# Kernel optimization log

Measured on AMD Instinct MI355X. Metric: run time of the kernel, lower is better.

## Reference

```python
import jax, jax.numpy as jnp
from jax import lax
import numpy as np

I, H, B, S = 512, 1024, 64, 512


def setup_inputs() -> dict:
    key = jax.random.key(0)
    ks = jax.random.split(key, 10)
    xav = lambda k, shape: jax.random.uniform(k, shape, jnp.float32, -1.0, 1.0) * jnp.sqrt(6.0 / (shape[0] + shape[1]))
    return {
        "x": jax.random.normal(ks[0], (B, S, I), jnp.float32),
        "wii": xav(ks[1], (I, H)), "bii": jnp.zeros((H,), jnp.float32),
        "whi": xav(ks[2], (H, H)), "bhi": jnp.zeros((H,), jnp.float32),
        "wif": xav(ks[3], (I, H)), "bif": jnp.zeros((H,), jnp.float32),
        "whf": xav(ks[4], (H, H)), "bhf": jnp.zeros((H,), jnp.float32),
        "wig": xav(ks[5], (I, H)), "big": jnp.zeros((H,), jnp.float32),
        "whg": xav(ks[6], (H, H)), "bhg": jnp.zeros((H,), jnp.float32),
        "wio": xav(ks[7], (I, H)), "bio": jnp.zeros((H,), jnp.float32),
        "who": xav(ks[8], (H, H)), "bho": jnp.zeros((H,), jnp.float32),
    }


def reference(x, wii, bii, whi, bhi, wif, bif, whf, bhf,
              wig, big, whg, bhg, wio, bio, who, bho):
    b, s, _ = x.shape
    h = wii.shape[1]
    # Fuse the four per-gate GEMMs into single (I,4H) / (H,4H) GEMMs — same math.
    Wx = jnp.concatenate([wii, wif, wig, wio], axis=1)   # (I, 4H)
    Wh = jnp.concatenate([whi, whf, whg, who], axis=1)   # (H, 4H)
    bb = jnp.concatenate([bii + bhi, bif + bhf, big + bhg, bio + bho])  # (4H,)
    xs = jnp.swapaxes(x, 0, 1)                            # (S, B, I)
    x_proj = jnp.einsum('sbi,ik->sbk', xs, Wx) + bb       # (S, B, 4H)

    def step(carry, xp):
        h_t, c_t = carry
        gates = xp + h_t @ Wh                             # (B, 4H)
        i_t, f_t, g_t, o_t = jnp.split(gates, 4, axis=-1)
        i_t = jax.nn.sigmoid(i_t)
        f_t = jax.nn.sigmoid(f_t)
        g_t = jnp.tanh(g_t)
        o_t = jax.nn.sigmoid(o_t)
        c_t = f_t * c_t + i_t * g_t
        h_t = o_t * jnp.tanh(c_t)
        return (h_t, c_t), None

    h0 = jnp.zeros((b, h), x.dtype)
    c0 = jnp.zeros((b, h), x.dtype)
    (h_T, c_T), _ = lax.scan(step, (h0, c0), x_proj)
    return (h_T, c_T)
```

## Files before the change

### kernel.cpp

```cpp
#include <hip/hip_runtime.h>
#include <hip/hip_bf16.h>
#include <stdint.h>

typedef __bf16 bf16_t;
typedef bf16_t bf16x8 __attribute__((ext_vector_type(8)));
typedef float  f32x4  __attribute__((ext_vector_type(4)));
typedef float  f32x16 __attribute__((ext_vector_type(16)));

#define I_DIM 512
#define H_DIM 1024
#define B_DIM 64
#define S_DIM 512
#define G4    4096
#define CHUNK 16
#define NCHUNK (S_DIM / CHUNK)
#define XPSLOT_ELEMS ((size_t)CHUNK * 64 * G4)

#define O_WXT   0x0000000ULL
#define O_WHTF  0x0400000ULL
#define O_BIAS  0x0C00000ULL
#define O_HBUF  0x0D00000ULL
#define O_BAR   0x0D40000ULL
#define O_XP    0x1200000ULL

#define XPD_IDX(c)  (2048 + (c) * 64)
#define CONS_IDX(c) (4096 + (c) * 64)
#define QF_BASE     6144

__device__ __forceinline__ float sigm(float x)      { return 1.f / (1.f + __expf(-x)); }
__device__ __forceinline__ float tanh_fast(float x) { return 1.f - 2.f / (__expf(2.f * x) + 1.f); }


__global__ void k_pack_wx(const float* __restrict__ w0, const float* __restrict__ w1,
                          const float* __restrict__ w2, const float* __restrict__ w3,
                          bf16_t* __restrict__ wxt) {
    int tid = blockIdx.x * 256 + threadIdx.x;
    int k = tid >> 12;
    int p = tid & 4095;
    int q = p >> 5, g = (p >> 3) & 3, jj = p & 7;
    int j = q * 8 + jj;
    const float* src = (g == 0) ? w0 : (g == 1) ? w1 : (g == 2) ? w2 : w3;
    wxt[(size_t)p * I_DIM + k] = (bf16_t)src[k * H_DIM + j];
}

__global__ void k_pack_whf(const float* __restrict__ w0, const float* __restrict__ w1,
                           const float* __restrict__ w2, const float* __restrict__ w3,
                           bf16_t* __restrict__ whtf) {
    int idx = blockIdx.x * 256 + threadIdx.x;
    int e    = idx & 7;
    int lane = (idx >> 3) & 63;
    int ks   = (idx >> 9) & 63;
    int q    = idx >> 15;
    int k = ks * 16 + (lane >> 5) * 8 + e;
    int c = lane & 31;
    int g = c >> 3, jj = c & 7;
    int j = q * 8 + jj;
    const float* src = (g == 0) ? w0 : (g == 1) ? w1 : (g == 2) ? w2 : w3;
    whtf[idx] = (bf16_t)src[k * H_DIM + j];
}

__global__ void k_pack_bias(const float* bi0, const float* bh0, const float* bi1, const float* bh1,
                            const float* bi2, const float* bh2, const float* bi3, const float* bh3,
                            float* __restrict__ bias) {
    int p = blockIdx.x * 256 + threadIdx.x;
    int q = p >> 5, g = (p >> 3) & 3, jj = p & 7;
    int j = q * 8 + jj;
    const float* a = (g == 0) ? bi0 : (g == 1) ? bi1 : (g == 2) ? bi2 : bi3;
    const float* b = (g == 0) ? bh0 : (g == 1) ? bh1 : (g == 2) ? bh2 : bh3;
    bias[p] = a[j] + b[j];
}

__global__ __launch_bounds__(256, 2) void k_mega(
    const float* __restrict__ x, const bf16_t* __restrict__ wxt,
    const float* __restrict__ bias, const bf16_t* __restrict__ whtf,
    bf16_t* __restrict__ xp, bf16_t* __restrict__ hbuf,
    float* __restrict__ out, uint32_t* __restrict__ bar)
{
    __shared__ float Pl[4][16][64];
    __shared__ __align__(16) bf16_t Hlds[256];
    __shared__ __align__(16) bf16_t Al[8 * 64 * 8];
    __shared__ __align__(16) bf16_t Bl[8 * 64 * 8];
    const int tid  = threadIdx.x;

    if (blockIdx.x >= 256) {
        const int xbid = blockIdx.x - 256;
        const int n0 = (xbid & 31) * 128;
        const int rt = (xbid >> 5) * 128;
        const int wv = tid >> 6;
        const int lane = tid & 63;
        const int mq = wv >> 1, nq = wv & 1;
        const int l15 = lane & 15, quad = lane >> 4;

        for (int sc = 0; sc < NCHUNK; ++sc) {
            if (sc >= 2) {
                if (tid == 0) {
                    while (__hip_atomic_load(&bar[CONS_IDX(sc - 2)], __ATOMIC_RELAXED,
                                             __HIP_MEMORY_SCOPE_AGENT) < 256u)
                        __builtin_amdgcn_s_sleep(2);
                }
                __syncthreads();
            }
            bf16_t* xps = xp + (size_t)(sc & 1) * XPSLOT_ELEMS;
            const int r_base = sc * (CHUNK * 64);

            f32x4 acc[4][4] = {};
            for (int kk = 0; kk < I_DIM; kk += 32) {
                __syncthreads();
                #pragma unroll
                for (int sidx = 0; sidx < 2; ++sidx) {
                    int s = tid + sidx * 256;
                    int mt = s >> 6, l = s & 63;
                    int m = l & 15, kb = (l >> 4) * 8;
                    int r = r_base + rt + mt * 16 + m;
                    int b = r & 63, si = r >> 6;
                    const float* gp = x + ((size_t)(b * S_DIM + si)) * I_DIM + kk + kb;
                    float4 v0 = *(const float4*)gp;
                    float4 v1 = *(const float4*)(gp + 4);
                    bf16x8 a;
                    a[0] = (bf16_t)v0.x; a[1] = (bf16_t)v0.y; a[2] = (bf16_t)v0.z; a[3] = (bf16_t)v0.w;
                    a[4] = (bf16_t)v1.x; a[5] = (bf16_t)v1.y; a[6] = (bf16_t)v1.z; a[7] = (bf16_t)v1.w;
                    *(bf16x8*)&Al[s * 8] = a;
                    bf16x8 bv = *(const bf16x8*)(wxt + (size_t)(n0 + mt * 16 + m) * I_DIM + kk + kb);
                    *(bf16x8*)&Bl[s * 8] = bv;
                }
                __syncthreads();
                bf16x8 af[4], bfr[4];
                #pragma unroll
                for (int mt = 0; mt < 4; ++mt) af[mt]  = *(bf16x8*)&Al[((mq * 4 + mt) * 64 + lane) * 8];
                #pragma unroll
                for (int nt = 0; nt < 4; ++nt) bfr[nt] = *(bf16x8*)&Bl[((nq * 4 + nt) * 64 + lane) * 8];
                #pragma unroll
                for (int mt = 0; mt < 4; ++mt)
                    #pragma unroll
                    for (int nt = 0; nt < 4; ++nt)
                        acc[mt][nt] = __builtin_amdgcn_mfma_f32_16x16x32_bf16(af[mt], bfr[nt], acc[mt][nt], 0, 0, 0);
            }
            #pragma unroll
            for (int nt = 0; nt < 4; ++nt) {
                int colg = n0 + nq * 64 + nt * 16 + l15;
                float bv = bias[colg];
                #pragma unroll
                for (int mt = 0; mt < 4; ++mt)
                    #pragma unroll
                    for (int r = 0; r < 4; ++r) {
                        int row = rt + mq * 64 + mt * 16 + quad * 4 + r;
                        bf16_t hb = (bf16_t)(acc[mt][nt][r] + bv);
                        __hip_atomic_store((uint16_t*)(xps + (size_t)row * G4 + colg),
                                           __builtin_bit_cast(unsigned short, hb),
                                           __ATOMIC_RELAXED, __HIP_MEMORY_SCOPE_AGENT);
                    }
            }
            asm volatile("s_waitcnt vmcnt(0)" ::: "memory");
            __syncthreads();
            if (tid == 0)
                __hip_atomic_fetch_add(&bar[XPD_IDX(sc)], 1u,
                                       __ATOMIC_RELAXED, __HIP_MEMORY_SCOPE_AGENT);
        }
        return;
    }

    const int w    = tid >> 6;
    const int lane = tid & 63;
    const int bid  = blockIdx.x;
    const int q    = bid & 127;
    const int bh   = bid >> 7;

    const int col  = lane & 31;
    const int ksel = lane >> 5;
    const int gt   = (lane >> 3) & 3;
    const int jj   = lane & 7;

    uint32_t* myflag = bar + QF_BASE + ((bh * 4 + (q >> 5)) << 6) + (q & 31);
    const uint32_t* qfb = bar + QF_BASE + ((bh * 4 + w) << 6);

    int rrow[4];
    #pragma unroll
    for (int e = 0; e < 4; ++e) rrow[e] = e + 8 * w + 4 * ksel;

    const bf16_t* bb = whtf + ((size_t)q << 15) + (w << 13) + (lane << 3);
    bf16x8 bfr[16];
    #pragma unroll
    for (int i = 0; i < 16; ++i) bfr[i] = *(const bf16x8*)(bb + i * 512);

    float cst[4] = {0.f, 0.f, 0.f, 0.f};

    const int abase = (bh << 15) + (w << 13) + (lane << 3);

    for (int c = 0; c < NCHUNK; ++c) {
        if (tid == 0) {
            while (__hip_atomic_load(&bar[XPD_IDX(c)], __ATOMIC_RELAXED,
                                     __HIP_MEMORY_SCOPE_AGENT) < 256u)
                __builtin_amdgcn_s_sleep(2);
        }
        __syncthreads();
        const uint16_t* xpc = (const uint16_t*)(xp + (size_t)(c & 1) * XPSLOT_ELEMS);

        for (int tl = 0; tl < CHUNK; ++tl) {
            const int t = c * CHUNK + tl;

            bf16_t xpr[4];
            #pragma unroll
            for (int e = 0; e < 4; ++e) {
                unsigned short v = __hip_atomic_load(
                    &xpc[(size_t)(tl * 64 + bh * 32 + rrow[e]) * G4 + q * 32 + col],
                    __ATOMIC_RELAXED, __HIP_MEMORY_SCOPE_AGENT);
                xpr[e] = __builtin_bit_cast(bf16_t, v);
            }

            if (t > 0) {
                const uint32_t target = (uint32_t)t;
                while (__hip_atomic_load(&qfb[lane & 31], __ATOMIC_RELAXED,
                                         __HIP_MEMORY_SCOPE_AGENT) < target) {}
            }
            asm volatile("" ::: "memory");

            const uint64_t* hsrc = (const uint64_t*)(hbuf + ((t & 1) << 16) + abase);
            uint64_t hl0[16], hl1[16];
            #pragma unroll
            for (int i = 0; i < 16; ++i) {
                hl0[i] = __hip_atomic_load(hsrc + i * 128,     __ATOMIC_RELAXED, __HIP_MEMORY_SCOPE_AGENT);
                hl1[i] = __hip_atomic_load(hsrc + i * 128 + 1, __ATOMIC_RELAXED, __HIP_MEMORY_SCOPE_AGENT);
            }

            struct U2 { uint64_t a, b; };
            f32x16 acc0 = {}, acc1 = {}, acc2 = {}, acc3 = {};
            #pragma unroll
            for (int i = 0; i < 16; i += 4) {
                U2 t0{hl0[i + 0], hl1[i + 0]};
                U2 t1{hl0[i + 1], hl1[i + 1]};
                U2 t2{hl0[i + 2], hl1[i + 2]};
                U2 t3{hl0[i + 3], hl1[i + 3]};
                acc0 = __builtin_amdgcn_mfma_f32_32x32x16_bf16(__builtin_bit_cast(bf16x8, t0), bfr[i + 0], acc0, 0, 0, 0);
                acc1 = __builtin_amdgcn_mfma_f32_32x32x16_bf16(__builtin_bit_cast(bf16x8, t1), bfr[i + 1], acc1, 0, 0, 0);
                acc2 = __builtin_amdgcn_mfma_f32_32x32x16_bf16(__builtin_bit_cast(bf16x8, t2), bfr[i + 2], acc2, 0, 0, 0);
                acc3 = __builtin_amdgcn_mfma_f32_32x32x16_bf16(__builtin_bit_cast(bf16x8, t3), bfr[i + 3], acc3, 0, 0, 0);
            }
            f32x16 accs = acc0 + acc1 + acc2 + acc3;

            #pragma unroll
            for (int e = 0; e < 16; ++e) Pl[w][e][lane] = accs[e];
            __syncthreads();

            #pragma unroll
            for (int e = 0; e < 4; ++e) {
                int eg = w * 4 + e;
                float pre = Pl[0][eg][lane] + Pl[1][eg][lane] + Pl[2][eg][lane] + Pl[3][eg][lane];
                pre += (float)xpr[e];
                float a = (gt == 2) ? tanh_fast(pre) : sigm(pre);

                float fv = __shfl_xor(a, 8, 64);
                float gv = __shfl_xor(a, 16, 64);
                float ov = __shfl_xor(a, 24, 64);
                if (gt == 0) {
                    float cn = fv * cst[e] + a * gv;
                    float hv = ov * tanh_fast(cn);
                    cst[e] = cn;
                    Hlds[rrow[e] * 8 + jj] = (bf16_t)hv;
                    if (t == S_DIM - 1) {
                        int rowg = bh * 32 + rrow[e];
                        int j = q * 8 + jj;
                        out[rowg * H_DIM + j] = hv;
                        out[65536 + rowg * H_DIM + j] = cn;
                    }
                }
            }
            __syncthreads();

            if (w == 0) {
                uint64_t v = *(const uint64_t*)&Hlds[lane * 4];
                uint64_t* hdst = (uint64_t*)hbuf + (((t + 1) & 1) << 14)
                               + (bh << 13) + (q << 6) + lane;
                __hip_atomic_store(hdst, v, __ATOMIC_RELAXED, __HIP_MEMORY_SCOPE_AGENT);
                if (t < S_DIM - 1) {
                    asm volatile("s_waitcnt vmcnt(0)" ::: "memory");
                    if (lane == 0)
                        __hip_atomic_store(myflag, (uint32_t)(t + 1),
                                           __ATOMIC_RELAXED, __HIP_MEMORY_SCOPE_AGENT);
                }
            }
        }

        if (tid == 0)
            __hip_atomic_fetch_add(&bar[CONS_IDX(c)], 1u,
                                   __ATOMIC_RELAXED, __HIP_MEMORY_SCOPE_AGENT);
    }
}

extern "C" void kernel_launch(void* const* d_in, const int* in_sizes, int n_in,
                              void* d_out, int out_size, void* d_ws, size_t ws_size,
                              hipStream_t stream) {
    const float* x   = (const float*)d_in[0];
    const float* wii = (const float*)d_in[1];
    const float* bii = (const float*)d_in[2];
    const float* whi = (const float*)d_in[3];
    const float* bhi = (const float*)d_in[4];
    const float* wif = (const float*)d_in[5];
    const float* bif = (const float*)d_in[6];
    const float* whf = (const float*)d_in[7];
    const float* bhf = (const float*)d_in[8];
    const float* wig = (const float*)d_in[9];
    const float* big = (const float*)d_in[10];
    const float* whg = (const float*)d_in[11];
    const float* bhg = (const float*)d_in[12];
    const float* wio = (const float*)d_in[13];
    const float* bio = (const float*)d_in[14];
    const float* who = (const float*)d_in[15];
    const float* bho = (const float*)d_in[16];

    char* ws = (char*)d_ws;
    bf16_t*   wxt  = (bf16_t*)(ws + O_WXT);
    bf16_t*   whtf = (bf16_t*)(ws + O_WHTF);
    float*    bias = (float*)(ws + O_BIAS);
    bf16_t*   hbuf = (bf16_t*)(ws + O_HBUF);
    uint32_t* bar  = (uint32_t*)(ws + O_BAR);
    bf16_t*   xp   = (bf16_t*)(ws + O_XP);

    hipMemsetAsync(hbuf, 0, 256 * 1024, stream);
    hipMemsetAsync(bar,  0, 32 * 1024, stream);

    k_pack_wx<<<8192, 256, 0, stream>>>(wii, wif, wig, wio, wxt);
    k_pack_whf<<<16384, 256, 0, stream>>>(whi, whf, whg, who, whtf);
    k_pack_bias<<<16, 256, 0, stream>>>(bii, bhi, bif, bhf, big, bhg, bio, bho, bias);

    float* out = (float*)d_out;
    void* args[] = { (void*)&x, (void*)&wxt, (void*)&bias, (void*)&whtf,
                     (void*)&xp, (void*)&hbuf, (void*)&out, (void*)&bar };
    hipError_t err = hipLaunchCooperativeKernel((const void*)k_mega, dim3(512), dim3(256),
                                                args, 0, stream);
    if (err != hipSuccess) {
        k_mega<<<512, 256, 0, stream>>>(x, wxt, bias, whtf, xp, hbuf, out, bar);
    }
}
```

Before: 3.848 ms.

## Pack four recurrent slices per 1024-thread block and use per-batch-half counter barrier

Grows the workgroups to 1024 threads. Each step block now holds four hidden-column slices, and each xproj block computes four GEMM tiles, which cuts the grid from 512 to 128 blocks. The per-timestep handshake changes from each wave polling 32 per-slice flags to one atomic counter per batch half that all 32 step blocks increment and spin on. The h loads are hoisted ahead of the x-projection loads because the barrier now completes before the next step starts. This aims to reduce the number of participants in the cross-block sync and its polling traffic, at the cost of a full block-wide barrier and the serialization of a single contended atomic every step.

```diff
diff --git a/kernel.cpp b/kernel.cpp
--- a/kernel.cpp
+++ b/kernel.cpp
@@ -15,6 +15,8 @@
 #define CHUNK 16
 #define NCHUNK (S_DIM / CHUNK)
 #define XPSLOT_ELEMS ((size_t)CHUNK * 64 * G4)
+#define STEP_WGS  64
+#define XPROJ_WGS 64
 
 #define O_WXT   0x0000000ULL
 #define O_WHTF  0x0400000ULL
@@ -25,7 +27,6 @@
 
 #define XPD_IDX(c)  (2048 + (c) * 64)
 #define CONS_IDX(c) (4096 + (c) * 64)
-#define QF_BASE     6144
 
 __device__ __forceinline__ float sigm(float x)      { return 1.f / (1.f + __expf(-x)); }
 __device__ __forceinline__ float tanh_fast(float x) { return 1.f - 2.f / (__expf(2.f * x) + 1.f); }
@@ -70,24 +71,26 @@
     bias[p] = a[j] + b[j];
 }
 
-__global__ __launch_bounds__(256, 2) void k_mega(
+__global__ __launch_bounds__(1024, 4) void k_mega(
     const float* __restrict__ x, const bf16_t* __restrict__ wxt,
     const float* __restrict__ bias, const bf16_t* __restrict__ whtf,
     bf16_t* __restrict__ xp, bf16_t* __restrict__ hbuf,
     float* __restrict__ out, uint32_t* __restrict__ bar)
 {
-    __shared__ float Pl[4][16][64];
-    __shared__ __align__(16) bf16_t Hlds[256];
-    __shared__ __align__(16) bf16_t Al[8 * 64 * 8];
-    __shared__ __align__(16) bf16_t Bl[8 * 64 * 8];
-    const int tid  = threadIdx.x;
-
-    if (blockIdx.x >= 256) {
-        const int xbid = blockIdx.x - 256;
-        const int n0 = (xbid & 31) * 128;
-        const int rt = (xbid >> 5) * 128;
-        const int wv = tid >> 6;
-        const int lane = tid & 63;
+    __shared__ __align__(16) unsigned char smem[68 * 1024];
+    const int tid = threadIdx.x;
+
+    if (blockIdx.x >= STEP_WGS) {
+        const int xbid = blockIdx.x - STEP_WGS;
+        const int qq   = tid >> 8;
+        const int qtid = tid & 255;
+        bf16_t* Al = (bf16_t*)(smem + qq * 16384);
+        bf16_t* Bl = Al + 4096;
+        const int tile = xbid * 4 + qq;
+        const int n0 = (tile & 31) * 128;
+        const int rt = (tile >> 5) * 128;
+        const int wv = qtid >> 6;
+        const int lane = qtid & 63;
         const int mq = wv >> 1, nq = wv & 1;
         const int l15 = lane & 15, quad = lane >> 4;
 
@@ -95,7 +98,7 @@
             if (sc >= 2) {
                 if (tid == 0) {
                     while (__hip_atomic_load(&bar[CONS_IDX(sc - 2)], __ATOMIC_RELAXED,
-                                             __HIP_MEMORY_SCOPE_AGENT) < 256u)
+                                             __HIP_MEMORY_SCOPE_AGENT) < (uint32_t)STEP_WGS)
                         __builtin_amdgcn_s_sleep(2);
                 }
                 __syncthreads();
@@ -108,7 +111,7 @@
                 __syncthreads();
                 #pragma unroll
                 for (int sidx = 0; sidx < 2; ++sidx) {
-                    int s = tid + sidx * 256;
+                    int s = qtid + sidx * 256;
                     int mt = s >> 6, l = s & 63;
                     int m = l & 15, kb = (l >> 4) * 8;
                     int r = r_base + rt + mt * 16 + m;
@@ -159,19 +162,23 @@
         return;
     }
 
-    const int w    = tid >> 6;
+    float (*Pl)[4][16][64] = (float (*)[4][16][64])smem;
+    bf16_t (*Hlds)[256]    = (bf16_t (*)[256])(smem + 65536);
+
+    const int wv   = tid >> 6;
+    const int g    = wv >> 2;
+    const int w    = wv & 3;
     const int lane = tid & 63;
     const int bid  = blockIdx.x;
-    const int q    = bid & 127;
-    const int bh   = bid >> 7;
+    const int q    = (bid & 31) * 4 + g;
+    const int bh   = bid >> 5;
 
     const int col  = lane & 31;
     const int ksel = lane >> 5;
     const int gt   = (lane >> 3) & 3;
     const int jj   = lane & 7;
 
-    uint32_t* myflag = bar + QF_BASE + ((bh * 4 + (q >> 5)) << 6) + (q & 31);
-    const uint32_t* qfb = bar + QF_BASE + ((bh * 4 + w) << 6);
+    uint32_t* cnt = bar + 1024 + (bh << 6);
 
     int rrow[4];
     #pragma unroll
@@ -189,7 +196,7 @@
     for (int c = 0; c < NCHUNK; ++c) {
         if (tid == 0) {
             while (__hip_atomic_load(&bar[XPD_IDX(c)], __ATOMIC_RELAXED,
-                                     __HIP_MEMORY_SCOPE_AGENT) < 256u)
+                                     __HIP_MEMORY_SCOPE_AGENT) < (uint32_t)XPROJ_WGS)
                 __builtin_amdgcn_s_sleep(2);
         }
         __syncthreads();
@@ -197,6 +204,14 @@
 
         for (int tl = 0; tl < CHUNK; ++tl) {
             const int t = c * CHUNK + tl;
+
+            const uint64_t* hsrc = (const uint64_t*)(hbuf + ((t & 1) << 16) + abase);
+            uint64_t hl0[16], hl1[16];
+            #pragma unroll
+            for (int i = 0; i < 16; ++i) {
+                hl0[i] = __hip_atomic_load(hsrc + i * 128,     __ATOMIC_RELAXED, __HIP_MEMORY_SCOPE_AGENT);
+                hl1[i] = __hip_atomic_load(hsrc + i * 128 + 1, __ATOMIC_RELAXED, __HIP_MEMORY_SCOPE_AGENT);
+            }
 
             bf16_t xpr[4];
             #pragma unroll
@@ -205,21 +220,6 @@
                     &xpc[(size_t)(tl * 64 + bh * 32 + rrow[e]) * G4 + q * 32 + col],
                     __ATOMIC_RELAXED, __HIP_MEMORY_SCOPE_AGENT);
                 xpr[e] = __builtin_bit_cast(bf16_t, v);
-            }
-
-            if (t > 0) {
-                const uint32_t target = (uint32_t)t;
-                while (__hip_atomic_load(&qfb[lane & 31], __ATOMIC_RELAXED,
-                                         __HIP_MEMORY_SCOPE_AGENT) < target) {}
-            }
-            asm volatile("" ::: "memory");
-
-            const uint64_t* hsrc = (const uint64_t*)(hbuf + ((t & 1) << 16) + abase);
-            uint64_t hl0[16], hl1[16];
-            #pragma unroll
-            for (int i = 0; i < 16; ++i) {
-                hl0[i] = __hip_atomic_load(hsrc + i * 128,     __ATOMIC_RELAXED, __HIP_MEMORY_SCOPE_AGENT);
-                hl1[i] = __hip_atomic_load(hsrc + i * 128 + 1, __ATOMIC_RELAXED, __HIP_MEMORY_SCOPE_AGENT);
             }
 
             struct U2 { uint64_t a, b; };
@@ -238,13 +238,14 @@
             f32x16 accs = acc0 + acc1 + acc2 + acc3;
 
             #pragma unroll
-            for (int e = 0; e < 16; ++e) Pl[w][e][lane] = accs[e];
+            for (int e = 0; e < 16; ++e) Pl[g][w][e][lane] = accs[e];
             __syncthreads();
 
             #pragma unroll
             for (int e = 0; e < 4; ++e) {
                 int eg = w * 4 + e;
-                float pre = Pl[0][eg][lane] + Pl[1][eg][lane] + Pl[2][eg][lane] + Pl[3][eg][lane];
+                float pre = Pl[g][0][eg][lane] + Pl[g][1][eg][lane]
+                          + Pl[g][2][eg][lane] + Pl[g][3][eg][lane];
                 pre += (float)xpr[e];
                 float a = (gt == 2) ? tanh_fast(pre) : sigm(pre);
 
@@ -255,7 +256,7 @@
                     float cn = fv * cst[e] + a * gv;
                     float hv = ov * tanh_fast(cn);
                     cst[e] = cn;
-                    Hlds[rrow[e] * 8 + jj] = (bf16_t)hv;
+                    Hlds[g][rrow[e] * 8 + jj] = (bf16_t)hv;
                     if (t == S_DIM - 1) {
                         int rowg = bh * 32 + rrow[e];
                         int j = q * 8 + jj;
@@ -267,16 +268,23 @@
             __syncthreads();
 
             if (w == 0) {
-                uint64_t v = *(const uint64_t*)&Hlds[lane * 4];
+                uint64_t v = *(const uint64_t*)&Hlds[g][lane * 4];
                 uint64_t* hdst = (uint64_t*)hbuf + (((t + 1) & 1) << 14)
                                + (bh << 13) + (q << 6) + lane;
                 __hip_atomic_store(hdst, v, __ATOMIC_RELAXED, __HIP_MEMORY_SCOPE_AGENT);
-                if (t < S_DIM - 1) {
+                if (t < S_DIM - 1)
                     asm volatile("s_waitcnt vmcnt(0)" ::: "memory");
-                    if (lane == 0)
-                        __hip_atomic_store(myflag, (uint32_t)(t + 1),
+            }
+            if (t < S_DIM - 1) {
+                __syncthreads();
+                if (tid == 0) {
+                    __hip_atomic_fetch_add(cnt, 1u,
                                            __ATOMIC_RELAXED, __HIP_MEMORY_SCOPE_AGENT);
+                    uint32_t target = (uint32_t)(32 * (t + 1));
+                    while (__hip_atomic_load(cnt, __ATOMIC_RELAXED,
+                                             __HIP_MEMORY_SCOPE_AGENT) < target) {}
                 }
+                __syncthreads();
             }
         }
 
@@ -325,9 +333,11 @@
     float* out = (float*)d_out;
     void* args[] = { (void*)&x, (void*)&wxt, (void*)&bias, (void*)&whtf,
                      (void*)&xp, (void*)&hbuf, (void*)&out, (void*)&bar };
-    hipError_t err = hipLaunchCooperativeKernel((const void*)k_mega, dim3(512), dim3(256),
+    hipError_t err = hipLaunchCooperativeKernel((const void*)k_mega,
+                                                dim3(STEP_WGS + XPROJ_WGS), dim3(1024),
                                                 args, 0, stream);
     if (err != hipSuccess) {
-        k_mega<<<512, 256, 0, stream>>>(x, wxt, bias, whtf, xp, hbuf, out, bar);
+        k_mega<<<STEP_WGS + XPROJ_WGS, 1024, 0, stream>>>(x, wxt, bias, whtf,
+                                                          xp, hbuf, out, bar);
     }
 }
```

Result: slower. 6.426 ms (+67.0%).

## Replace per-step flag barrier with tagged hidden-state words polled directly

Applied to the files above, without the earlier changes.

The per-step producer flags and the spin on them are removed. Each bf16 hidden value is now stored in a 32-bit word together with a 16-bit timestep tag, and consumers poll the h buffer itself until every tag matches the current step. This drops the store-wait-then-flag round trip on the serial recurrence path. In exchange the h buffer doubles in size, every load carries twice the bytes, and values must be unpacked before the MFMA.

```diff
diff --git a/kernel.cpp b/kernel.cpp
--- a/kernel.cpp
+++ b/kernel.cpp
@@ -6,6 +6,7 @@
 typedef bf16_t bf16x8 __attribute__((ext_vector_type(8)));
 typedef float  f32x4  __attribute__((ext_vector_type(4)));
 typedef float  f32x16 __attribute__((ext_vector_type(16)));
+typedef unsigned int u32x4 __attribute__((ext_vector_type(4)));
 
 #define I_DIM 512
 #define H_DIM 1024
@@ -20,12 +21,11 @@
 #define O_WHTF  0x0400000ULL
 #define O_BIAS  0x0C00000ULL
 #define O_HBUF  0x0D00000ULL
-#define O_BAR   0x0D40000ULL
+#define O_BAR   0x0D80000ULL
 #define O_XP    0x1200000ULL
 
 #define XPD_IDX(c)  (2048 + (c) * 64)
 #define CONS_IDX(c) (4096 + (c) * 64)
-#define QF_BASE     6144
 
 __device__ __forceinline__ float sigm(float x)      { return 1.f / (1.f + __expf(-x)); }
 __device__ __forceinline__ float tanh_fast(float x) { return 1.f - 2.f / (__expf(2.f * x) + 1.f); }
@@ -73,7 +73,7 @@
 __global__ __launch_bounds__(256, 2) void k_mega(
     const float* __restrict__ x, const bf16_t* __restrict__ wxt,
     const float* __restrict__ bias, const bf16_t* __restrict__ whtf,
-    bf16_t* __restrict__ xp, bf16_t* __restrict__ hbuf,
+    bf16_t* __restrict__ xp, uint32_t* __restrict__ hbuf,
     float* __restrict__ out, uint32_t* __restrict__ bar)
 {
     __shared__ float Pl[4][16][64];
@@ -170,9 +170,6 @@
     const int gt   = (lane >> 3) & 3;
     const int jj   = lane & 7;
 
-    uint32_t* myflag = bar + QF_BASE + ((bh * 4 + (q >> 5)) << 6) + (q & 31);
-    const uint32_t* qfb = bar + QF_BASE + ((bh * 4 + w) << 6);
-
     int rrow[4];
     #pragma unroll
     for (int e = 0; e < 4; ++e) rrow[e] = e + 8 * w + 4 * ksel;
@@ -184,7 +181,8 @@
 
     float cst[4] = {0.f, 0.f, 0.f, 0.f};
 
-    const int abase = (bh << 15) + (w << 13) + (lane << 3);
+    const int cbase = (bh << 14) + (w << 12) + (lane << 2);
+    const int pbase = ((bh << 13) + (q << 6) + lane) << 1;
 
     for (int c = 0; c < NCHUNK; ++c) {
         if (tid == 0) {
@@ -197,6 +195,7 @@
 
         for (int tl = 0; tl < CHUNK; ++tl) {
             const int t = c * CHUNK + tl;
+            const uint32_t tag = (uint32_t)t & 0xffffu;
 
             bf16_t xpr[4];
             #pragma unroll
@@ -207,33 +206,44 @@
                 xpr[e] = __builtin_bit_cast(bf16_t, v);
             }
 
-            if (t > 0) {
-                const uint32_t target = (uint32_t)t;
-                while (__hip_atomic_load(&qfb[lane & 31], __ATOMIC_RELAXED,
-                                         __HIP_MEMORY_SCOPE_AGENT) < target) {}
-            }
-            asm volatile("" ::: "memory");
-
-            const uint64_t* hsrc = (const uint64_t*)(hbuf + ((t & 1) << 16) + abase);
-            uint64_t hl0[16], hl1[16];
-            #pragma unroll
-            for (int i = 0; i < 16; ++i) {
-                hl0[i] = __hip_atomic_load(hsrc + i * 128,     __ATOMIC_RELAXED, __HIP_MEMORY_SCOPE_AGENT);
-                hl1[i] = __hip_atomic_load(hsrc + i * 128 + 1, __ATOMIC_RELAXED, __HIP_MEMORY_SCOPE_AGENT);
-            }
-
-            struct U2 { uint64_t a, b; };
+            const uint64_t* hsrc = (const uint64_t*)hbuf + ((t & 1) << 15) + cbase;
+            u32x4 af[16];
+            for (;;) {
+                int ok = 1;
+                #pragma unroll
+                for (int ib = 0; ib < 4; ++ib) {
+                    uint64_t d[16];
+                    #pragma unroll
+                    for (int ii = 0; ii < 4; ++ii) {
+                        const uint64_t* p = hsrc + (ib * 4 + ii) * 256;
+                        d[ii * 4 + 0] = __hip_atomic_load(p + 0, __ATOMIC_RELAXED, __HIP_MEMORY_SCOPE_AGENT);
+                        d[ii * 4 + 1] = __hip_atomic_load(p + 1, __ATOMIC_RELAXED, __HIP_MEMORY_SCOPE_AGENT);
+                        d[ii * 4 + 2] = __hip_atomic_load(p + 2, __ATOMIC_RELAXED, __HIP_MEMORY_SCOPE_AGENT);
+                        d[ii * 4 + 3] = __hip_atomic_load(p + 3, __ATOMIC_RELAXED, __HIP_MEMORY_SCOPE_AGENT);
+                    }
+                    #pragma unroll
+                    for (int ii = 0; ii < 4; ++ii) {
+                        u32x4 v;
+                        #pragma unroll
+                        for (int k2 = 0; k2 < 4; ++k2) {
+                            uint64_t dk = d[ii * 4 + k2];
+                            uint32_t lo = (uint32_t)dk, hi = (uint32_t)(dk >> 32);
+                            v[k2] = (lo >> 16) | (hi & 0xffff0000u);
+                            ok &= (int)((lo & 0xffffu) == tag);
+                        }
+                        af[ib * 4 + ii] = v;
+                    }
+                }
+                if (__all(ok)) break;
+            }
+
             f32x16 acc0 = {}, acc1 = {}, acc2 = {}, acc3 = {};
             #pragma unroll
             for (int i = 0; i < 16; i += 4) {
-                U2 t0{hl0[i + 0], hl1[i + 0]};
-                U2 t1{hl0[i + 1], hl1[i + 1]};
-                U2 t2{hl0[i + 2], hl1[i + 2]};
-                U2 t3{hl0[i + 3], hl1[i + 3]};
-                acc0 = __builtin_amdgcn_mfma_f32_32x32x16_bf16(__builtin_bit_cast(bf16x8, t0), bfr[i + 0], acc0, 0, 0, 0);
-                acc1 = __builtin_amdgcn_mfma_f32_32x32x16_bf16(__builtin_bit_cast(bf16x8, t1), bfr[i + 1], acc1, 0, 0, 0);
-                acc2 = __builtin_amdgcn_mfma_f32_32x32x16_bf16(__builtin_bit_cast(bf16x8, t2), bfr[i + 2], acc2, 0, 0, 0);
-                acc3 = __builtin_amdgcn_mfma_f32_32x32x16_bf16(__builtin_bit_cast(bf16x8, t3), bfr[i + 3], acc3, 0, 0, 0);
+                acc0 = __builtin_amdgcn_mfma_f32_32x32x16_bf16(__builtin_bit_cast(bf16x8, af[i + 0]), bfr[i + 0], acc0, 0, 0, 0);
+                acc1 = __builtin_amdgcn_mfma_f32_32x32x16_bf16(__builtin_bit_cast(bf16x8, af[i + 1]), bfr[i + 1], acc1, 0, 0, 0);
+                acc2 = __builtin_amdgcn_mfma_f32_32x32x16_bf16(__builtin_bit_cast(bf16x8, af[i + 2]), bfr[i + 2], acc2, 0, 0, 0);
+                acc3 = __builtin_amdgcn_mfma_f32_32x32x16_bf16(__builtin_bit_cast(bf16x8, af[i + 3]), bfr[i + 3], acc3, 0, 0, 0);
             }
             f32x16 accs = acc0 + acc1 + acc2 + acc3;
 
@@ -267,16 +277,16 @@
             __syncthreads();
 
             if (w == 0) {
-                uint64_t v = *(const uint64_t*)&Hlds[lane * 4];
-                uint64_t* hdst = (uint64_t*)hbuf + (((t + 1) & 1) << 14)
-                               + (bh << 13) + (q << 6) + lane;
-                __hip_atomic_store(hdst, v, __ATOMIC_RELAXED, __HIP_MEMORY_SCOPE_AGENT);
-                if (t < S_DIM - 1) {
-                    asm volatile("s_waitcnt vmcnt(0)" ::: "memory");
-                    if (lane == 0)
-                        __hip_atomic_store(myflag, (uint32_t)(t + 1),
-                                           __ATOMIC_RELAXED, __HIP_MEMORY_SCOPE_AGENT);
-                }
+                const uint32_t ntag = (uint32_t)(t + 1) & 0xffffu;
+                uint32_t b01 = *(const uint32_t*)&Hlds[lane * 4];
+                uint32_t b23 = *(const uint32_t*)&Hlds[lane * 4 + 2];
+                uint64_t d0 = ((uint64_t)((b01 & 0xffff0000u) | ntag) << 32)
+                            | ((b01 << 16) | ntag);
+                uint64_t d1 = ((uint64_t)((b23 & 0xffff0000u) | ntag) << 32)
+                            | ((b23 << 16) | ntag);
+                uint64_t* hdst = (uint64_t*)hbuf + (((t + 1) & 1) << 15) + pbase;
+                __hip_atomic_store(hdst,     d0, __ATOMIC_RELAXED, __HIP_MEMORY_SCOPE_AGENT);
+                __hip_atomic_store(hdst + 1, d1, __ATOMIC_RELAXED, __HIP_MEMORY_SCOPE_AGENT);
             }
         }
 
@@ -311,11 +321,11 @@
     bf16_t*   wxt  = (bf16_t*)(ws + O_WXT);
     bf16_t*   whtf = (bf16_t*)(ws + O_WHTF);
     float*    bias = (float*)(ws + O_BIAS);
-    bf16_t*   hbuf = (bf16_t*)(ws + O_HBUF);
+    uint32_t* hbuf = (uint32_t*)(ws + O_HBUF);
     uint32_t* bar  = (uint32_t*)(ws + O_BAR);
     bf16_t*   xp   = (bf16_t*)(ws + O_XP);
 
-    hipMemsetAsync(hbuf, 0, 256 * 1024, stream);
+    hipMemsetAsync(hbuf, 0, 512 * 1024, stream);
     hipMemsetAsync(bar,  0, 32 * 1024, stream);
 
     k_pack_wx<<<8192, 256, 0, stream>>>(wii, wif, wig, wio, wxt);
```

Measured after the change: 6.352 ms. +65.1%, slower.
